# Kernel tuning notes

Measured on AMD Instinct MI355X. Metric: run time of the kernel, lower is better.

## Reference

```python
import jax, jax.numpy as jnp
import numpy as np

B, S, D = 2, 2048, 2048
H, KVH = 16, 4
HD = D // H          # 128 head dim
KVD = KVH * HD       # 512
BASE = 10000.0
EPS = 1.1920929e-07  # float32 eps, matches torch F.rms_norm default


def setup_inputs() -> dict:
    key = jax.random.key(0)
    ks = jax.random.split(key, 9)
    sd = 1.0 / np.sqrt(D)
    x = jax.random.normal(ks[0], (B, S, D), jnp.float32)
    Wq = jax.random.normal(ks[1], (D, D), jnp.float32) * sd
    bq = jnp.zeros((D,), jnp.float32)
    Wk = jax.random.normal(ks[2], (KVD, D), jnp.float32) * sd
    bk = jnp.zeros((KVD,), jnp.float32)
    Wv = jax.random.normal(ks[3], (KVD, D), jnp.float32) * sd
    bv = jnp.zeros((KVD,), jnp.float32)
    Wo = jax.random.normal(ks[4], (D, D), jnp.float32) * sd
    bo = jnp.zeros((D,), jnp.float32)
    q_gain = jnp.ones((H,), jnp.float32)
    return {"x": x, "Wq": Wq, "bq": bq, "Wk": Wk, "bk": bk,
            "Wv": Wv, "bv": bv, "Wo": Wo, "bo": bo, "q_gain": q_gain}


def _rms_norm(t):
    return t * jax.lax.rsqrt(jnp.mean(t * t, axis=-1, keepdims=True) + EPS)


def _rope_tables(s, dtype):
    inv_freq = 1.0 / (BASE ** (jnp.arange(0, HD, 2, dtype=jnp.float32) / HD))  # [HD/2]
    t = jnp.arange(s, dtype=jnp.float32)
    freqs = jnp.outer(t, inv_freq)                       # [s, HD/2]
    cos = jnp.cos(freqs)[None, None].astype(dtype)       # [1,1,s,HD/2]
    sin = jnp.sin(freqs)[None, None].astype(dtype)
    return cos, sin


def _apply_rope(t, cos, sin):
    half = t.shape[-1] // 2
    t1, t2 = t[..., :half], t[..., half:]
    return jnp.concatenate([t1 * cos + t2 * sin, -t1 * sin + t2 * cos], axis=-1)


def reference(x, Wq, bq, Wk, bk, Wv, bv, Wo, bo, q_gain):
    b, s, d = x.shape
    q = (jnp.einsum('bsd,ed->bse', x, Wq) + bq).reshape(b, s, H, HD).transpose(0, 2, 1, 3)
    k = (jnp.einsum('bsd,ed->bse', x, Wk) + bk).reshape(b, s, KVH, HD).transpose(0, 2, 1, 3)
    v = (jnp.einsum('bsd,ed->bse', x, Wv) + bv).reshape(b, s, KVH, HD).transpose(0, 2, 1, 3)
    # QK RMSNorm (no learned weight)
    q = _rms_norm(q)
    k = _rms_norm(k)
    # RoPE over full head dim (rope_dims=0 path)
    cos, sin = _rope_tables(s, q.dtype)
    q = _apply_rope(q, cos, sin)
    k = _apply_rope(k, cos, sin)
    # per-head gain on q
    q = q * q_gain[None, :, None, None]
    # GQA: repeat kv heads
    rep = H // KVH
    k = jnp.repeat(k, rep, axis=1)
    v = jnp.repeat(v, rep, axis=1)
    scale = HD ** -0.5
    attn = jnp.einsum('bhqd,bhkd->bhqk', q * scale, k)   # [b,H,s,s]
    causal = jnp.tril(jnp.ones((s, s), dtype=bool))
    attn = jnp.where(causal[None, None], attn, -jnp.inf)
    attn = jax.nn.softmax(attn, axis=-1)
    out = jnp.einsum('bhqk,bhkd->bqhd', attn, v).reshape(b, s, d)
    return jnp.einsum('bsd,ed->bse', out, Wo) + bo
```

## Files before the change

kernel.cpp:

```cpp
#include <hip/hip_runtime.h>
#include <hip/hip_bf16.h>

typedef __hip_bfloat16 bf16;
typedef unsigned short u16;
typedef short short8 __attribute__((ext_vector_type(8)));
typedef float f32x4  __attribute__((ext_vector_type(4)));

static __device__ __forceinline__ float b2f(u16 u) {
    union { unsigned int i; float f; } c; c.i = (unsigned int)u << 16; return c.f;
}

static __device__ __forceinline__ float ldf(const void* p, size_t i, int isbf16) {
    return isbf16 ? __bfloat162float(((const bf16*)p)[i]) : ((const float*)p)[i];
}
static __device__ __forceinline__ void stf(void* p, size_t i, float v, int isbf16) {
    if (isbf16) ((bf16*)p)[i] = __float2bfloat16(v);
    else        ((float*)p)[i] = v;
}

static __device__ __forceinline__ unsigned packf(float v) {
    unsigned ub = __float_as_uint(v);
    unsigned uh = ub & 0xFFFF0000u;
    float r = v - __uint_as_float(uh);
    return uh | (__float_as_uint(r) >> 16);
}
static __device__ __forceinline__ float unpackf(unsigned u) {
    return __uint_as_float(u & 0xFFFF0000u) + __uint_as_float(u << 16);
}

static __device__ __forceinline__ void upk8(uint4 a, uint4 b, short8& h, short8& l) {
    h = (short8){(short)(a.x >> 16), (short)(a.y >> 16), (short)(a.z >> 16), (short)(a.w >> 16),
                 (short)(b.x >> 16), (short)(b.y >> 16), (short)(b.z >> 16), (short)(b.w >> 16)};
    l = (short8){(short)(a.x), (short)(a.y), (short)(a.z), (short)(a.w),
                 (short)(b.x), (short)(b.y), (short)(b.z), (short)(b.w)};
}

static __device__ __forceinline__ void splitf8(float4 a, float4 b, short8& h, short8& l) {
    float vv[8] = {a.x, a.y, a.z, a.w, b.x, b.y, b.z, b.w};
    unsigned hh[8], ll[8];
#pragma unroll
    for (int j = 0; j < 8; j++) {
        unsigned ub = __float_as_uint(vv[j]);
        unsigned uh = ub & 0xFFFF0000u;
        float r = vv[j] - __uint_as_float(uh);
        hh[j] = uh >> 16;
        ll[j] = __float_as_uint(r) >> 16;
    }
    h = (short8){(short)hh[0], (short)hh[1], (short)hh[2], (short)hh[3],
                 (short)hh[4], (short)hh[5], (short)hh[6], (short)hh[7]};
    l = (short8){(short)ll[0], (short)ll[1], (short)ll[2], (short)ll[3],
                 (short)ll[4], (short)ll[5], (short)ll[6], (short)ll[7]};
}

static __device__ __forceinline__ float4 u2f4(uint4 a) {
    return (float4){__uint_as_float(a.x), __uint_as_float(a.y),
                    __uint_as_float(a.z), __uint_as_float(a.w)};
}
static __device__ __forceinline__ short8 u4_s8(uint4 a) {
    return (short8){(short)(a.x & 0xFFFF), (short)(a.x >> 16),
                    (short)(a.y & 0xFFFF), (short)(a.y >> 16),
                    (short)(a.z & 0xFFFF), (short)(a.z >> 16),
                    (short)(a.w & 0xFFFF), (short)(a.w >> 16)};
}

template<int MODE>
static __device__ __forceinline__ void load_any(const void* P, size_t e, int f, uint4* r) {
    if (MODE == 2) {
        const uint4* p = (const uint4*)((const unsigned*)P + e);
        r[0] = p[0]; r[1] = p[1]; r[2] = p[2]; r[3] = p[3];
    } else if (f == 0) {
        const uint4* p = (const uint4*)((const float*)P + e);
        r[0] = p[0]; r[1] = p[1]; r[2] = p[2]; r[3] = p[3];
    } else {
        const uint4* p = (const uint4*)((const u16*)P + e);
        r[0] = p[0]; r[1] = p[1];
        r[2] = (uint4){0, 0, 0, 0}; r[3] = (uint4){0, 0, 0, 0};
    }
}
template<int MODE>
static __device__ __forceinline__ void conv_any(const uint4* r, int f,
        short8& h0, short8& h1, short8& l0, short8& l1) {
    if (MODE == 2) {
        upk8(r[0], r[1], h0, l0);
        upk8(r[2], r[3], h1, l1);
    } else if (f == 0) {
        splitf8(u2f4(r[0]), u2f4(r[1]), h0, l0);
        splitf8(u2f4(r[2]), u2f4(r[3]), h1, l1);
    } else {
        h0 = u4_s8(r[0]); h1 = u4_s8(r[1]);
        l0 = (short8){0,0,0,0,0,0,0,0};
        l1 = (short8){0,0,0,0,0,0,0,0};
    }
}

static __device__ __forceinline__ void async_copy16(const void* g, void* l) {
    __builtin_amdgcn_global_load_lds((const __attribute__((address_space(1))) void*)g,
                                     (__attribute__((address_space(3))) void*)l, 16, 0, 0);
}

__global__ void detect_dtype(const unsigned short* __restrict__ x, int n, int* __restrict__ flag)
{
    __shared__ int cnt;
    if (threadIdx.x == 0) cnt = 0;
    __syncthreads();
    int local = 0;
    for (int i = threadIdx.x; i < n; i += blockDim.x) {
        const unsigned int e = (x[i] >> 7) & 0xFF;
        if (e >= 134u) local++;
    }
    atomicAdd(&cnt, local);
    __syncthreads();
    if (threadIdx.x == 0) *flag = (cnt >= 32) ? 0 : 1;
}

__global__ __launch_bounds__(256)
void split_x(const void* __restrict__ x, u16* __restrict__ Xh, u16* __restrict__ Xl,
             const int* __restrict__ flagp)
{
    const int f = *flagp;
    const size_t i = ((size_t)blockIdx.x * 256 + threadIdx.x) * 8;
    if (f == 0) {
        const float4* p = (const float4*)((const float*)x + i);
        short8 h, l;
        splitf8(p[0], p[1], h, l);
        *(short8*)(Xh + i) = h;
        *(short8*)(Xl + i) = l;
    } else {
        *(short8*)(Xh + i) = *(const short8*)((const u16*)x + i);
        *(short8*)(Xl + i) = (short8){0,0,0,0,0,0,0,0};
    }
}

template<int AM, int BM, int OUT, int BROW>
static __device__ __forceinline__ void gemm_core(
    const void* __restrict__ Aa, const void* __restrict__ Ab,
    const void* __restrict__ Ba, const void* __restrict__ Bb,
    const void* __restrict__ bias, void* __restrict__ Ca,
    int N, int K, int f, int bx, int by, u16* sm)
{
    u16* AhT = sm;
    u16* AlT = sm + 4096;
    u16* WhT = sm + 8192;
    u16* WlT = sm + 12288;

    const int t = threadIdx.x;
    const int w = t >> 6, lane = t & 63;
    const int wm = w >> 1, wn = w & 1;
    const int lr = lane & 15, quad = lane >> 4;
    const int bm = by * 128, bn = bx * 128;
    const int arow = lane >> 2;
    const int acol = (lane & 3) * 8;
    const int srow = t >> 1, scol = (t & 1) * 16;

    f32x4 acc[4][4];
#pragma unroll
    for (int i = 0; i < 4; i++)
#pragma unroll
        for (int j = 0; j < 4; j++) acc[i][j] = (f32x4){0.f, 0.f, 0.f, 0.f};

    uint4 ra[4], rb[4];
    const size_t aBase = (size_t)(bm + srow) * K + scol;
    const size_t bBase = (size_t)(bn + srow) * K + scol;
    if (AM != 1) load_any<AM>(Aa, aBase, f, ra);
    if (BM != 1) load_any<BM>(Ba, bBase, f, rb);

    for (int k0 = 0; k0 < K; k0 += 32) {
        __syncthreads();
        if (AM == 1) {
#pragma unroll
            for (int c = 2 * w; c < 2 * w + 2; c++) {
                const int row = c * 16 + arow;
                async_copy16((const u16*)Aa + (size_t)(bm + row) * K + k0 + acol, &AhT[c * 512]);
                async_copy16((const u16*)Ab + (size_t)(bm + row) * K + k0 + acol, &AlT[c * 512]);
            }
        } else {
            short8 h0, h1, l0, l1;
            conv_any<AM>(ra, f, h0, h1, l0, l1);
            const int o = srow * 32 + scol;
            *(short8*)&AhT[o] = h0; *(short8*)&AhT[o + 8] = h1;
            *(short8*)&AlT[o] = l0; *(short8*)&AlT[o + 8] = l1;
        }
        if (BM == 1) {
#pragma unroll
            for (int c = 2 * w; c < 2 * w + 2; c++) {
                const int row = c * 16 + arow;
                async_copy16((const u16*)Ba + (size_t)(bn + row) * K + k0 + acol, &WhT[c * 512]);
                async_copy16((const u16*)Bb + (size_t)(bn + row) * K + k0 + acol, &WlT[c * 512]);
            }
        } else {
            short8 h0, h1, l0, l1;
            conv_any<BM>(rb, f, h0, h1, l0, l1);
            const int o = srow * 32 + scol;
            *(short8*)&WhT[o] = h0; *(short8*)&WhT[o + 8] = h1;
            *(short8*)&WlT[o] = l0; *(short8*)&WlT[o + 8] = l1;
        }
        __syncthreads();
        if (k0 + 32 < K) {
            if (AM != 1) load_any<AM>(Aa, aBase + k0 + 32, f, ra);
            if (BM != 1) load_any<BM>(Ba, bBase + k0 + 32, f, rb);
        }

        short8 avh[4], avl[4], bvh[4], bvl[4];
#pragma unroll
        for (int i = 0; i < 4; i++) {
            const int o = (wm * 64 + i * 16 + lr) * 32 + quad * 8;
            avh[i] = *(const short8*)&AhT[o];
            avl[i] = *(const short8*)&AlT[o];
        }
#pragma unroll
        for (int j = 0; j < 4; j++) {
            const int o = (wn * 64 + j * 16 + lr) * 32 + quad * 8;
            bvh[j] = *(const short8*)&WhT[o];
            bvl[j] = *(const short8*)&WlT[o];
        }
        __builtin_amdgcn_s_setprio(1);
#pragma unroll
        for (int i = 0; i < 4; i++)
#pragma unroll
            for (int j = 0; j < 4; j++) {
                acc[i][j] = __builtin_amdgcn_mfma_f32_16x16x32_bf16(avl[i], bvh[j], acc[i][j], 0, 0, 0);
                acc[i][j] = __builtin_amdgcn_mfma_f32_16x16x32_bf16(avh[i], bvl[j], acc[i][j], 0, 0, 0);
                acc[i][j] = __builtin_amdgcn_mfma_f32_16x16x32_bf16(avh[i], bvh[j], acc[i][j], 0, 0, 0);
            }
        __builtin_amdgcn_s_setprio(0);
    }

#pragma unroll
    for (int j = 0; j < 4; j++) {
        const int col = bn + wn * 64 + j * 16 + lr;
        const float bc = BROW ? 0.f : ldf(bias, col, f);
#pragma unroll
        for (int i = 0; i < 4; i++) {
            const int row0 = bm + wm * 64 + i * 16 + quad * 4;
#pragma unroll
            for (int r = 0; r < 4; r++) {
                const int row = row0 + r;
                const float bb = BROW ? ldf(bias, row, f) : bc;
                const float val = acc[i][j][r] + bb;
                const size_t idx = (size_t)row * N + col;
                if (OUT == 1) ((unsigned*)Ca)[idx] = packf(val);
                else          stf(Ca, idx, val, f);
            }
        }
    }
}

__global__ __launch_bounds__(256, 3)
void gemm_qkv(const u16* __restrict__ Xh, const u16* __restrict__ Xl,
              const void* __restrict__ Wq, const void* __restrict__ bq, unsigned* __restrict__ Qp,
              const void* __restrict__ Wk, const void* __restrict__ bk, unsigned* __restrict__ Kp,
              const void* __restrict__ Wv, const void* __restrict__ bv, unsigned* __restrict__ Vtp,
              const int* __restrict__ flagp)
{
    __shared__ __align__(16) u16 sm[16384];
    const int f = *flagp;
    const int id = blockIdx.x;
    if (id < 512) {
        gemm_core<1, 0, 1, 0>(Xh, Xl, Wq, nullptr, bq, Qp,
                              2048, 2048, f, id & 15, id >> 4, sm);
    } else if (id < 640) {
        const int v = id - 512;
        gemm_core<1, 0, 1, 0>(Xh, Xl, Wk, nullptr, bk, Kp,
                              512, 2048, f, v & 3, v >> 2, sm);
    } else {
        const int v = id - 640;
        gemm_core<0, 1, 1, 1>(Wv, nullptr, Xh, Xl, bv, Vtp,
                              4096, 2048, f, v >> 2, v & 3, sm);
    }
}

__global__ __launch_bounds__(256, 2)
void gemm_o(const unsigned* __restrict__ Cp, const void* __restrict__ Wo,
            const void* __restrict__ bo, void* __restrict__ out,
            const int* __restrict__ flagp)
{
    __shared__ __align__(16) u16 sm[16384];
    gemm_core<2, 0, 2, 0>(Cp, nullptr, Wo, nullptr, bo, out,
                          2048, 2048, *flagp, blockIdx.x & 15, blockIdx.x >> 4, sm);
}

__global__ __launch_bounds__(64)
void norm_rope_pk(unsigned* __restrict__ buf, const void* __restrict__ gain,
                  int nheads, float scale, const int* __restrict__ flagp)
{
    const int id = blockIdx.x;
    const int h  = id % nheads;
    const int bs = id / nheads;
    const int s  = bs & 2047;
    unsigned* v = buf + (size_t)bs * nheads * 128 + h * 128;
    const int i = threadIdx.x;

    float t1 = unpackf(v[i]);
    float t2 = unpackf(v[i + 64]);
    float ss = t1 * t1 + t2 * t2;
#pragma unroll
    for (int off = 32; off >= 1; off >>= 1) ss += __shfl_xor(ss, off);
    const float r = rsqrtf(ss * (1.0f / 128.0f) + 1.1920929e-07f);
    t1 *= r; t2 *= r;

    const float inv_freq = exp2f(-(float)i * 0.20762050593046014f);
    const float ph = (float)s * inv_freq;
    float sn, cs;
    __sincosf(ph, &sn, &cs);

    float g = scale;
    if (gain) g *= ldf(gain, h, *flagp);

    v[i]      = packf((t1 * cs + t2 * sn) * g);
    v[i + 64] = packf((-t1 * sn + t2 * cs) * g);
}

__global__ __launch_bounds__(256, 2)
void attn3(const unsigned* __restrict__ Qp, const unsigned* __restrict__ Kp,
           const unsigned* __restrict__ Vtp, unsigned* __restrict__ Cp)
{
    const int S = 2048, D = 2048, KVD = 512, MT = 4096;

    __shared__ __align__(16) u16 Kh[64 * 128], Kl[64 * 128];
    __shared__ __align__(16) u16 Vh[128 * 64], Vl[128 * 64];
    __shared__ __align__(16) u16 Ps[4][16][72];

    const int t = threadIdx.x, w = t >> 6, lane = t & 63;
    const int lr = lane & 15, quad = lane >> 4;
    const int h = blockIdx.y, b = blockIdx.z;
    const int kvh = h >> 2;

    const int qt0 = blockIdx.x;
    const int qt1 = 31 - blockIdx.x;
    const int nt0 = qt0 + 1, nt1 = qt1 + 1;
    const int total = nt0 + nt1;

    const int kr = t >> 2, kq = t & 3;
    const int vd = t >> 1, vh2 = t & 1;
    const unsigned* kg = Kp + (size_t)(b * S + kr) * KVD + kvh * 128 + kq * 32;
    const unsigned* vg = Vtp + (size_t)(kvh * 128 + vd) * MT + b * S + vh2 * 32;
    char* KhB = (char*)Kh; char* KlB = (char*)Kl;
    char* VhB = (char*)Vh; char* VlB = (char*)Vl;

    uint4 kv[8], vv[8];
#define ISSUE_KV(K0)                                                     \
    do {                                                                 \
        _Pragma("unroll")                                                \
        for (int u = 0; u < 8; u++) {                                    \
            kv[u] = *(const uint4*)(kg + (size_t)(K0) * KVD + u * 4);    \
            vv[u] = *(const uint4*)(vg + (K0) + u * 4);                  \
        }                                                                \
    } while (0)

    short8 qh[4], ql[4];
    f32x4 acc[8];
    float mreg[4], lreg[4];
    int q0 = 0, nt = nt0;

    ISSUE_KV(0);

    for (int it = 0; it < total; it++) {
        const int item = (it >= nt0) ? 1 : 0;
        const int kt = item ? (it - nt0) : it;
        if (kt == 0) {
            nt = item ? nt1 : nt0;
            q0 = (item ? qt1 : qt0) * 64;
            const unsigned* qs = Qp + (size_t)(b * S + q0 + w * 16 + lr) * D + h * 128;
#pragma unroll
            for (int kk = 0; kk < 4; kk++) {
                const uint4* p = (const uint4*)(qs + kk * 32 + quad * 8);
                upk8(p[0], p[1], qh[kk], ql[kk]);
            }
#pragma unroll
            for (int dt = 0; dt < 8; dt++) acc[dt] = (f32x4){0.f, 0.f, 0.f, 0.f};
#pragma unroll
            for (int r = 0; r < 4; r++) { mreg[r] = -1e30f; lreg[r] = 0.f; }
        }
        const int k0 = kt * 64;

        __syncthreads();
#pragma unroll
        for (int u2 = 0; u2 < 4; u2++) {
            short8 hh, ll;
            upk8(kv[2 * u2], kv[2 * u2 + 1], hh, ll);
            const int ko = (kr * 256 + kq * 64 + u2 * 16) ^ ((kr & 7) << 4);
            *(short8*)(KhB + ko) = hh;
            *(short8*)(KlB + ko) = ll;
            upk8(vv[2 * u2], vv[2 * u2 + 1], hh, ll);
            const int vo = (vd * 128 + vh2 * 64 + u2 * 16) ^ ((vd & 7) << 4);
            *(short8*)(VhB + vo) = hh;
            *(short8*)(VlB + vo) = ll;
        }
        __syncthreads();

        if (it + 1 < total) {
            const int nk0 = (it + 1 >= nt0) ? (it + 1 - nt0) * 64 : (it + 1) * 64;
            ISSUE_KV(nk0);
        }

        f32x4 sacc[4];
#pragma unroll
        for (int ct = 0; ct < 4; ct++) sacc[ct] = (f32x4){0.f, 0.f, 0.f, 0.f};
#pragma unroll
        for (int ks = 0; ks < 4; ks++) {
            short8 kbh[4], kbl[4];
#pragma unroll
            for (int ct = 0; ct < 4; ct++) {
                const int row = ct * 16 + lr;
                const int off = (row * 256 + ks * 64 + quad * 16) ^ ((row & 7) << 4);
                kbh[ct] = *(const short8*)(KhB + off);
                kbl[ct] = *(const short8*)(KlB + off);
            }
            __builtin_amdgcn_s_setprio(1);
#pragma unroll
            for (int ct = 0; ct < 4; ct++) {
                sacc[ct] = __builtin_amdgcn_mfma_f32_16x16x32_bf16(ql[ks], kbh[ct], sacc[ct], 0, 0, 0);
                sacc[ct] = __builtin_amdgcn_mfma_f32_16x16x32_bf16(qh[ks], kbl[ct], sacc[ct], 0, 0, 0);
                sacc[ct] = __builtin_amdgcn_mfma_f32_16x16x32_bf16(qh[ks], kbh[ct], sacc[ct], 0, 0, 0);
            }
            __builtin_amdgcn_s_setprio(0);
        }

        const bool diag = (kt == nt - 1);
        float p[4][4];
#pragma unroll
        for (int r = 0; r < 4; r++) {
            const int qg = q0 + w * 16 + quad * 4 + r;
            float s0 = sacc[0][r], s1 = sacc[1][r], s2 = sacc[2][r], s3 = sacc[3][r];
            if (diag) {
                if (k0 +  0 + lr > qg) s0 = -1e30f;
                if (k0 + 16 + lr > qg) s1 = -1e30f;
                if (k0 + 32 + lr > qg) s2 = -1e30f;
                if (k0 + 48 + lr > qg) s3 = -1e30f;
            }
            float mt = fmaxf(fmaxf(s0, s1), fmaxf(s2, s3));
#pragma unroll
            for (int off = 1; off < 16; off <<= 1) mt = fmaxf(mt, __shfl_xor(mt, off));
            const float mnew  = fmaxf(mreg[r], mt);
            const float alpha = __expf(mreg[r] - mnew);
            p[r][0] = (s0 <= -1e29f) ? 0.f : __expf(s0 - mnew);
            p[r][1] = (s1 <= -1e29f) ? 0.f : __expf(s1 - mnew);
            p[r][2] = (s2 <= -1e29f) ? 0.f : __expf(s2 - mnew);
            p[r][3] = (s3 <= -1e29f) ? 0.f : __expf(s3 - mnew);
            float ps = p[r][0] + p[r][1] + p[r][2] + p[r][3];
#pragma unroll
            for (int off = 1; off < 16; off <<= 1) ps += __shfl_xor(ps, off);
            lreg[r] = lreg[r] * alpha + ps;
            mreg[r] = mnew;
#pragma unroll
            for (int dt = 0; dt < 8; dt++) acc[dt][r] *= alpha;
        }

#pragma unroll
        for (int r = 0; r < 4; r++)
#pragma unroll
            for (int ct = 0; ct < 4; ct++)
                Ps[w][quad * 4 + r][ct * 16 + lr] = (u16)(__float_as_uint(p[r][ct]) >> 16);
#pragma unroll
        for (int ks2 = 0; ks2 < 2; ks2++) {
            const short8 pa = *(const short8*)((const char*)&Ps[w][lr][0] + ks2 * 64 + quad * 16);
            __builtin_amdgcn_s_setprio(1);
#pragma unroll
            for (int dt = 0; dt < 8; dt++) {
                const int vrow = dt * 16 + lr;
                const int off = (vrow * 128 + ks2 * 64 + quad * 16) ^ ((vrow & 7) << 4);
                const short8 vbh = *(const short8*)(VhB + off);
                const short8 vbl = *(const short8*)(VlB + off);
                acc[dt] = __builtin_amdgcn_mfma_f32_16x16x32_bf16(pa, vbh, acc[dt], 0, 0, 0);
                acc[dt] = __builtin_amdgcn_mfma_f32_16x16x32_bf16(pa, vbl, acc[dt], 0, 0, 0);
            }
            __builtin_amdgcn_s_setprio(0);
        }
#pragma unroll
        for (int r = 0; r < 4; r++)
#pragma unroll
            for (int ct = 0; ct < 4; ct++) {
                const unsigned ub = __float_as_uint(p[r][ct]);
                const unsigned uh = ub & 0xFFFF0000u;
                const float rr = p[r][ct] - __uint_as_float(uh);
                Ps[w][quad * 4 + r][ct * 16 + lr] = (u16)(__float_as_uint(rr) >> 16);
            }
#pragma unroll
        for (int ks2 = 0; ks2 < 2; ks2++) {
            const short8 pa = *(const short8*)((const char*)&Ps[w][lr][0] + ks2 * 64 + quad * 16);
            __builtin_amdgcn_s_setprio(1);
#pragma unroll
            for (int dt = 0; dt < 8; dt++) {
                const int vrow = dt * 16 + lr;
                const int off = (vrow * 128 + ks2 * 64 + quad * 16) ^ ((vrow & 7) << 4);
                const short8 vbh = *(const short8*)(VhB + off);
                acc[dt] = __builtin_amdgcn_mfma_f32_16x16x32_bf16(pa, vbh, acc[dt], 0, 0, 0);
            }
            __builtin_amdgcn_s_setprio(0);
        }

        if (kt == nt - 1) {
#pragma unroll
            for (int r = 0; r < 4; r++) {
                const float inv = 1.0f / lreg[r];
                unsigned* dst = Cp + (size_t)(b * S + q0 + w * 16 + quad * 4 + r) * D + h * 128 + lr;
#pragma unroll
                for (int dt = 0; dt < 8; dt++)
                    dst[dt * 16] = packf(acc[dt][r] * inv);
            }
        }
    }
#undef ISSUE_KV
}

extern "C" void kernel_launch(void* const* d_in, const int* in_sizes, int n_in,
                              void* d_out, int out_size, void* d_ws, size_t ws_size,
                              hipStream_t stream)
{
    const void* x  = d_in[0];
    const void* Wq = d_in[1];
    const void* bq = d_in[2];
    const void* Wk = d_in[3];
    const void* bk = d_in[4];
    const void* Wv = d_in[5];
    const void* bv = d_in[6];
    const void* Wo = d_in[7];
    const void* bo = d_in[8];
    const void* qg = d_in[9];

    const int B = 2, S = 2048, D = 2048, H = 16, KVH = 4, KVD = 512;
    const int M = B * S;

    unsigned* Qp  = (unsigned*)d_ws;
    unsigned* Kp  = Qp + (size_t)M * D;
    unsigned* Vtp = Kp + (size_t)M * KVD;
    unsigned* Cp  = Vtp + (size_t)KVD * M;
    int* flag = (int*)(Cp + (size_t)M * D);
    u16* CXh = (u16*)Cp;
    u16* CXl = CXh + (size_t)M * D;

    detect_dtype<<<1, 256, 0, stream>>>((const unsigned short*)x, 16384, flag);

    split_x<<<(M * D) / (256 * 8), 256, 0, stream>>>(x, CXh, CXl, flag);

    gemm_qkv<<<768, 256, 0, stream>>>(CXh, CXl, Wq, bq, Qp,
                                      Wk, bk, Kp, Wv, bv, Vtp, flag);

    norm_rope_pk<<<M * H, 64, 0, stream>>>(Qp, qg, H, 0.08838834764831845f, flag);
    norm_rope_pk<<<M * KVH, 64, 0, stream>>>(Kp, nullptr, KVH, 1.0f, flag);

    attn3<<<dim3(16, H, B), 256, 0, stream>>>(Qp, Kp, Vtp, Cp);

    gemm_o<<<512, 256, 0, stream>>>(Cp, Wo, bo, d_out, flag);
}
```

Baseline: 673.6 us.

## Store attention output as split hi/lo planes and reorder MFMA chains

The attention kernel now writes its output as two separate bf16 planes (high and low halves) instead of packed 32-bit words. The output GEMM then consumes them through the split-input path already used for Q/K/V, which avoids unpacking inside its loads, and its occupancy hint is raised from 2 to 3 blocks per SM. The MFMA loops in the GEMM core and in attention are reordered so consecutive instructions write different accumulators, breaking back-to-back dependencies on the same accumulator. The higher occupancy target may force register spills, and the scattered 16-bit stores in the epilogue may be less efficient than the packed 32-bit stores.

Result: faster. 659.8 us (-2.0%).

```diff
diff --git a/kernel.cpp b/kernel.cpp
--- a/kernel.cpp
+++ b/kernel.cpp
@@ -217,11 +217,18 @@
 #pragma unroll
         for (int i = 0; i < 4; i++)
 #pragma unroll
-            for (int j = 0; j < 4; j++) {
+            for (int j = 0; j < 4; j++)
                 acc[i][j] = __builtin_amdgcn_mfma_f32_16x16x32_bf16(avl[i], bvh[j], acc[i][j], 0, 0, 0);
+#pragma unroll
+        for (int i = 0; i < 4; i++)
+#pragma unroll
+            for (int j = 0; j < 4; j++)
                 acc[i][j] = __builtin_amdgcn_mfma_f32_16x16x32_bf16(avh[i], bvl[j], acc[i][j], 0, 0, 0);
+#pragma unroll
+        for (int i = 0; i < 4; i++)
+#pragma unroll
+            for (int j = 0; j < 4; j++)
                 acc[i][j] = __builtin_amdgcn_mfma_f32_16x16x32_bf16(avh[i], bvh[j], acc[i][j], 0, 0, 0);
-            }
         __builtin_amdgcn_s_setprio(0);
     }
 
@@ -269,13 +276,13 @@
     }
 }
 
-__global__ __launch_bounds__(256, 2)
-void gemm_o(const unsigned* __restrict__ Cp, const void* __restrict__ Wo,
-            const void* __restrict__ bo, void* __restrict__ out,
-            const int* __restrict__ flagp)
+__global__ __launch_bounds__(256, 3)
+void gemm_o(const u16* __restrict__ Ch, const u16* __restrict__ Cl,
+            const void* __restrict__ Wo, const void* __restrict__ bo,
+            void* __restrict__ out, const int* __restrict__ flagp)
 {
     __shared__ __align__(16) u16 sm[16384];
-    gemm_core<2, 0, 2, 0>(Cp, nullptr, Wo, nullptr, bo, out,
+    gemm_core<1, 0, 2, 0>(Ch, Cl, Wo, nullptr, bo, out,
                           2048, 2048, *flagp, blockIdx.x & 15, blockIdx.x >> 4, sm);
 }
 
@@ -312,7 +319,8 @@
 
 __global__ __launch_bounds__(256, 2)
 void attn3(const unsigned* __restrict__ Qp, const unsigned* __restrict__ Kp,
-           const unsigned* __restrict__ Vtp, unsigned* __restrict__ Cp)
+           const unsigned* __restrict__ Vtp,
+           u16* __restrict__ Chg, u16* __restrict__ Clg)
 {
     const int S = 2048, D = 2048, KVD = 512, MT = 4096;
 
@@ -408,11 +416,14 @@
             }
             __builtin_amdgcn_s_setprio(1);
 #pragma unroll
-            for (int ct = 0; ct < 4; ct++) {
+            for (int ct = 0; ct < 4; ct++)
                 sacc[ct] = __builtin_amdgcn_mfma_f32_16x16x32_bf16(ql[ks], kbh[ct], sacc[ct], 0, 0, 0);
+#pragma unroll
+            for (int ct = 0; ct < 4; ct++)
                 sacc[ct] = __builtin_amdgcn_mfma_f32_16x16x32_bf16(qh[ks], kbl[ct], sacc[ct], 0, 0, 0);
+#pragma unroll
+            for (int ct = 0; ct < 4; ct++)
                 sacc[ct] = __builtin_amdgcn_mfma_f32_16x16x32_bf16(qh[ks], kbh[ct], sacc[ct], 0, 0, 0);
-            }
             __builtin_amdgcn_s_setprio(0);
         }
 
@@ -460,8 +471,13 @@
                 const int vrow = dt * 16 + lr;
                 const int off = (vrow * 128 + ks2 * 64 + quad * 16) ^ ((vrow & 7) << 4);
                 const short8 vbh = *(const short8*)(VhB + off);
+                acc[dt] = __builtin_amdgcn_mfma_f32_16x16x32_bf16(pa, vbh, acc[dt], 0, 0, 0);
+            }
+#pragma unroll
+            for (int dt = 0; dt < 8; dt++) {
+                const int vrow = dt * 16 + lr;
+                const int off = (vrow * 128 + ks2 * 64 + quad * 16) ^ ((vrow & 7) << 4);
                 const short8 vbl = *(const short8*)(VlB + off);
-                acc[dt] = __builtin_amdgcn_mfma_f32_16x16x32_bf16(pa, vbh, acc[dt], 0, 0, 0);
                 acc[dt] = __builtin_amdgcn_mfma_f32_16x16x32_bf16(pa, vbl, acc[dt], 0, 0, 0);
             }
             __builtin_amdgcn_s_setprio(0);
@@ -493,10 +509,15 @@
 #pragma unroll
             for (int r = 0; r < 4; r++) {
                 const float inv = 1.0f / lreg[r];
-                unsigned* dst = Cp + (size_t)(b * S + q0 + w * 16 + quad * 4 + r) * D + h * 128 + lr;
-#pragma unroll
-                for (int dt = 0; dt < 8; dt++)
-                    dst[dt * 16] = packf(acc[dt][r] * inv);
+                const size_t base = (size_t)(b * S + q0 + w * 16 + quad * 4 + r) * D + h * 128 + lr;
+#pragma unroll
+                for (int dt = 0; dt < 8; dt++) {
+                    const float val = acc[dt][r] * inv;
+                    const unsigned ub = __float_as_uint(val);
+                    const unsigned uh = ub & 0xFFFF0000u;
+                    Chg[base + dt * 16] = (u16)(uh >> 16);
+                    Clg[base + dt * 16] = (u16)(__float_as_uint(val - __uint_as_float(uh)) >> 16);
+                }
             }
         }
     }
@@ -539,7 +560,7 @@
     norm_rope_pk<<<M * H, 64, 0, stream>>>(Qp, qg, H, 0.08838834764831845f, flag);
     norm_rope_pk<<<M * KVH, 64, 0, stream>>>(Kp, nullptr, KVH, 1.0f, flag);
 
-    attn3<<<dim3(16, H, B), 256, 0, stream>>>(Qp, Kp, Vtp, Cp);
-
-    gemm_o<<<512, 256, 0, stream>>>(Cp, Wo, bo, d_out, flag);
-}
+    attn3<<<dim3(16, H, B), 256, 0, stream>>>(Qp, Kp, Vtp, CXh, CXl);
+
+    gemm_o<<<512, 256, 0, stream>>>(CXh, CXl, Wo, bo, d_out, flag);
+}
```
